# Optimization experiments

Hardware: AMD Instinct MI355X
Metric: run time of the kernel (lower is better)

The kernel has to match this reference:

```python
import jax, jax.numpy as jnp
import numpy as np

N_NODES = 100000
N_EDGES = 800000
NODE_F = 32
EDGE_F = 16
HID = 128
EPS = 1e-5


def _bn(h, g, b):
    # BatchNorm1d in training mode: biased batch stats over dim 0
    m = h.mean(axis=0)
    v = jnp.mean((h - m) ** 2, axis=0)
    return (h - m) * jax.lax.rsqrt(v + EPS) * g + b


def _sage(x, src, dst, Wl, bl, Wr):
    # PyG SAGEConv (mean aggr): lin_l(mean_{j->i} x_j) + lin_r(x_i)
    s = jax.ops.segment_sum(x[src], dst, num_segments=N_NODES)
    cnt = jax.ops.segment_sum(jnp.ones((src.shape[0], 1), x.dtype), dst, num_segments=N_NODES)
    mean = s / jnp.maximum(cnt, 1.0)
    return mean @ Wl + bl + x @ Wr


def setup_inputs() -> dict:
    key = jax.random.key(0)
    ks = jax.random.split(key, 32)

    def lin(k, fi, fo):
        return jax.random.normal(k, (fi, fo), jnp.float32) / np.sqrt(fi)

    inp = {
        'x': jax.random.normal(ks[0], (N_NODES, NODE_F), jnp.float32),
        'edge_index': jax.random.randint(ks[1], (2, N_EDGES), 0, N_NODES),
        'edge_attr': jax.random.normal(ks[2], (N_EDGES, EDGE_F), jnp.float32),
        'edge_source': jax.random.randint(ks[3], (N_EDGES,), 0, N_NODES),
        'edge_target': jax.random.randint(ks[4], (N_EDGES,), 0, N_NODES),
        'W1l': lin(ks[5], NODE_F, HID), 'b1': jnp.zeros((HID,), jnp.float32), 'W1r': lin(ks[6], NODE_F, HID),
        'W2l': lin(ks[7], HID, HID), 'b2': jnp.zeros((HID,), jnp.float32), 'W2r': lin(ks[8], HID, HID),
        'bn1_g': jnp.ones((HID,), jnp.float32), 'bn1_b': jnp.zeros((HID,), jnp.float32),
        'bn2_g': jnp.ones((HID,), jnp.float32), 'bn2_b': jnp.zeros((HID,), jnp.float32),
        'We': lin(ks[9], EDGE_F, HID), 'be': jnp.zeros((HID,), jnp.float32),
        'bne_g': jnp.ones((HID,), jnp.float32), 'bne_b': jnp.zeros((HID,), jnp.float32),
        'Wm1': lin(ks[10], 3 * HID, HID), 'bm1': jnp.zeros((HID,), jnp.float32),
        'bnm_g': jnp.ones((HID,), jnp.float32), 'bnm_b': jnp.zeros((HID,), jnp.float32),
        'Wm2': lin(ks[11], HID, HID // 2), 'bm2': jnp.zeros((HID // 2,), jnp.float32),
        'Wm3': lin(ks[12], HID // 2, 1), 'bm3': jnp.zeros((1,), jnp.float32),
    }
    return inp


def reference(x, edge_index, edge_attr, edge_source, edge_target,
              W1l, b1, W1r, W2l, b2, W2r, bn1_g, bn1_b, bn2_g, bn2_b,
              We, be, bne_g, bne_b, Wm1, bm1, bnm_g, bnm_b, Wm2, bm2, Wm3, bm3):
    src, dst = edge_index[0], edge_index[1]
    h = jax.nn.relu(_bn(_sage(x, src, dst, W1l, b1, W1r), bn1_g, bn1_b))  # dropout = identity (eval)
    h = jax.nn.relu(_bn(_sage(h, src, dst, W2l, b2, W2r), bn2_g, bn2_b))
    ef = _bn(jax.nn.relu(edge_attr @ We + be), bne_g, bne_b)  # Linear->ReLU->BN->Dropout(id)
    z = jnp.concatenate([h[edge_source], h[edge_target], ef], axis=1)  # [E, 3*HID]
    z = _bn(jax.nn.relu(z @ Wm1 + bm1), bnm_g, bnm_b)
    z = jax.nn.relu(z @ Wm2 + bm2)
    return (z @ Wm3 + bm3).squeeze(-1)
```

## Files before the change

kernel.cpp:

```cpp
#include <hip/hip_runtime.h>
#include <hip/hip_bf16.h>

#define NN 100000
#define NE 800000
#define SCAN_NB 98

typedef __attribute__((ext_vector_type(8))) short bf16x8;
typedef __attribute__((ext_vector_type(4))) float f32x4;

__device__ __forceinline__ short f2b(float f) {
    unsigned u = __float_as_uint(f);
    unsigned r = (u + 0x7fffu + ((u >> 16) & 1u)) >> 16;
    return (short)r;
}
__device__ __forceinline__ float b2f(short s) {
    return __uint_as_float(((unsigned)(unsigned short)s) << 16);
}
__device__ __forceinline__ unsigned cvt2(float a, float b) {
    unsigned r;
    asm("v_cvt_pk_bf16_f32 %0, %1, %2" : "=v"(r) : "v"(a), "v"(b));
    return r;
}
__device__ __forceinline__ float blo(unsigned u) { return __uint_as_float(u << 16); }
__device__ __forceinline__ float bhi(unsigned u) { return __uint_as_float(u & 0xffff0000u); }

__global__ __launch_bounds__(256) void k_prep_hist(
    const float* __restrict__ We, const float* __restrict__ Wm1,
    const float* __restrict__ W2l, const float* __restrict__ W2r,
    short* __restrict__ WteT, short* __restrict__ WmsT,
    short* __restrict__ WmdT, short* __restrict__ W2cT,
    const int* __restrict__ ei, int* __restrict__ deg)
{
    int b = blockIdx.x;
    int tid = threadIdx.x;
    if (b >= 5) {
        int e = (b - 5) * 256 + tid;
        if (e < NE) atomicAdd(&deg[ei[NE + e]], 1);
        return;
    }
    if (tid >= 128) return;
    int j = tid;
    if (b == 0) {
        for (int k = 0; k < 32; k++)
            WteT[j * 32 + k] = (k < 16) ? f2b(We[k * 128 + j]) : (short)0;
    } else if (b == 1) {
        for (int k = 0; k < 128; k++) WmsT[j * 128 + k] = f2b(Wm1[k * 128 + j]);
    } else if (b == 2) {
        for (int k = 0; k < 128; k++) WmdT[j * 128 + k] = f2b(Wm1[(128 + k) * 128 + j]);
    } else if (b == 3) {
        for (int k = 0; k < 128; k++) W2cT[j * 256 + k] = f2b(W2l[k * 128 + j]);
    } else {
        for (int k = 0; k < 128; k++) W2cT[j * 256 + 128 + k] = f2b(W2r[k * 128 + j]);
    }
}

__global__ __launch_bounds__(1024) void k_scan_a(const int* __restrict__ deg,
    int* __restrict__ tmp, int* __restrict__ bsum)
{
    __shared__ int sh[1024];
    int t = threadIdx.x, b = blockIdx.x;
    int idx = b * 1024 + t;
    int v = (idx < NN) ? deg[idx] : 0;
    sh[t] = v;
    __syncthreads();
    for (int ofs = 1; ofs < 1024; ofs <<= 1) {
        int u = (t >= ofs) ? sh[t - ofs] : 0;
        __syncthreads();
        sh[t] += u;
        __syncthreads();
    }
    if (idx < NN) tmp[idx] = sh[t] - v;
    if (t == 1023) bsum[b] = sh[1023];
}

__global__ void k_scan_b(const int* __restrict__ bsum, int* __restrict__ boff,
    int* __restrict__ rowptr)
{
    if (threadIdx.x == 0) {
        int acc = 0;
        for (int i = 0; i < SCAN_NB; i++) { boff[i] = acc; acc += bsum[i]; }
        rowptr[NN] = acc;
    }
}

__global__ __launch_bounds__(1024) void k_scan_c(const int* __restrict__ tmp,
    const int* __restrict__ boff, int* __restrict__ rowptr, int* __restrict__ wp)
{
    int b = blockIdx.x, t = threadIdx.x;
    int idx = b * 1024 + t;
    if (idx < NN) {
        int v = boff[b] + tmp[idx];
        rowptr[idx] = v; wp[idx] = v;
    }
}

#define SCAT_NB 3125
__global__ __launch_bounds__(256) void k_scat_e0(
    const int* __restrict__ ei, int* __restrict__ wp, int* __restrict__ elist,
    const float* __restrict__ ea, const short* __restrict__ WteT, const float* __restrict__ be,
    float* __restrict__ ssum, float* __restrict__ ssq)
{
    const int tid = threadIdx.x;
    if (blockIdx.x < SCAT_NB) {
        int e = blockIdx.x * 256 + tid;
        if (e < NE) {
            int d = ei[NE + e];
            int pos = atomicAdd(&wp[d], 1);
            elist[pos] = ei[e];
        }
        return;
    }
    __shared__ float sRed[2][128];
    const int wave = tid >> 6, lane = tid & 63;
    const int quad = lane >> 4, ln = lane & 15;
    const int waveM = wave >> 1, waveN = wave & 1;
    const int colbase = 64 * waveN, row16 = 16 * waveM;
    if (tid < 128) { sRed[0][tid] = 0.f; sRed[1][tid] = 0.f; }

    bf16x8 bWe[4];
    float bec[4];
    #pragma unroll
    for (int nt = 0; nt < 4; nt++) {
        bWe[nt] = *(const bf16x8*)(WteT + (colbase + nt * 16 + ln) * 32 + quad * 8);
        bec[nt] = be[colbase + nt * 16 + ln];
    }
    float s1[4] = {0,0,0,0}, s2[4] = {0,0,0,0};
    f32x4 zero = {0.f, 0.f, 0.f, 0.f};
    __syncthreads();

    const int G = gridDim.x - SCAT_NB;
    const int NT = NE / 32;
    float4 fe0 = {0,0,0,0}, fe1 = {0,0,0,0};
    int t = blockIdx.x - SCAT_NB;
    if (t < NT && quad < 2) {
        const float* p = ea + (size_t)(t * 32 + row16 + ln) * 16 + quad * 8;
        fe0 = *(const float4*)p; fe1 = *(const float4*)(p + 4);
    }
    for (; t < NT; t += G) {
        bf16x8 aE;
        if (quad < 2) {
            uint4 uw;
            uw.x = cvt2(fe0.x, fe0.y); uw.y = cvt2(fe0.z, fe0.w);
            uw.z = cvt2(fe1.x, fe1.y); uw.w = cvt2(fe1.z, fe1.w);
            aE = *(bf16x8*)&uw;
        } else {
            #pragma unroll
            for (int i = 0; i < 8; i++) aE[i] = 0;
        }
        int t1 = t + G;
        if (t1 < NT && quad < 2) {
            const float* p = ea + (size_t)(t1 * 32 + row16 + ln) * 16 + quad * 8;
            fe0 = *(const float4*)p; fe1 = *(const float4*)(p + 4);
        }
        f32x4 tacc[4];
        #pragma unroll
        for (int nt = 0; nt < 4; nt++)
            tacc[nt] = __builtin_amdgcn_mfma_f32_16x16x32_bf16(aE, bWe[nt], zero, 0, 0, 0);
        #pragma unroll
        for (int nt = 0; nt < 4; nt++)
            #pragma unroll
            for (int r = 0; r < 4; r++) {
                float v = fmaxf(tacc[nt][r] + bec[nt], 0.f);
                s1[nt] += v; s2[nt] += v * v;
            }
    }
    #pragma unroll
    for (int nt = 0; nt < 4; nt++) {
        float a1 = s1[nt], a2 = s2[nt];
        a1 += __shfl_down(a1, 32); a1 += __shfl_down(a1, 16);
        a2 += __shfl_down(a2, 32); a2 += __shfl_down(a2, 16);
        if (quad == 0) {
            atomicAdd(&sRed[0][colbase + nt * 16 + ln], a1);
            atomicAdd(&sRed[1][colbase + nt * 16 + ln], a2);
        }
    }
    __syncthreads();
    if (tid < 128) {
        atomicAdd(&ssum[tid], sRed[0][tid]);
        atomicAdd(&ssq[tid],  sRed[1][tid]);
    }
}

__global__ __launch_bounds__(256) void k_gagg1f(const float* __restrict__ x,
    const int* __restrict__ rowptr, const int* __restrict__ elist, float* __restrict__ meanX,
    const float* __restrict__ essum, const float* __restrict__ essq,
    const float* __restrict__ bne_g, const float* __restrict__ bne_b,
    const float* __restrict__ Wm1, const float* __restrict__ bm1,
    short* __restrict__ W1pT, float* __restrict__ bm1p)
{
    if (blockIdx.x == NN / 8) {
        __shared__ float sa[128], scc[128];
        int tid = threadIdx.x;
        if (tid < 128) {
            float m = essum[tid] / (float)NE;
            float var = essq[tid] / (float)NE - m * m;
            float rs = rsqrtf(var + 1e-5f);
            float a = bne_g[tid] * rs;
            sa[tid] = a; scc[tid] = bne_b[tid] - m * a;
        }
        __syncthreads();
        if (tid < 128) {
            float acc = bm1[tid];
            for (int k = 0; k < 128; k++) {
                float w = Wm1[(256 + k) * 128 + tid];
                W1pT[tid * 128 + k] = f2b(sa[k] * w);
                acc += scc[k] * w;
            }
            bm1p[tid] = acc;
        }
        return;
    }
    int n = blockIdx.x * 8 + (threadIdx.x >> 5);
    int j = threadIdx.x & 31;
    int b = rowptr[n], e = rowptr[n + 1];
    float acc = 0.f;
    int i = b;
    for (; i + 4 <= e; i += 4) {
        int s0 = elist[i], s1 = elist[i + 1], s2 = elist[i + 2], s3 = elist[i + 3];
        float a0 = x[(size_t)s0 * 32 + j];
        float a1 = x[(size_t)s1 * 32 + j];
        float a2 = x[(size_t)s2 * 32 + j];
        float a3 = x[(size_t)s3 * 32 + j];
        acc += (a0 + a1) + (a2 + a3);
    }
    for (; i < e; i++) acc += x[(size_t)elist[i] * 32 + j];
    float inv = (e > b) ? 1.0f / (float)(e - b) : 1.0f;
    meanX[(size_t)n * 32 + j] = acc * inv;
}

__global__ __launch_bounds__(256) void k_gagg2(const short* __restrict__ h1b,
    const int* __restrict__ rowptr, const int* __restrict__ elist,
    const float* __restrict__ ssum1, const float* __restrict__ ssq1,
    const float* __restrict__ g1, const float* __restrict__ b1g, short* __restrict__ m2b)
{
    int n = blockIdx.x * 8 + (threadIdx.x >> 5);
    int c0 = (threadIdx.x & 31) * 4;
    float sc[4], sh[4];
    #pragma unroll
    for (int i = 0; i < 4; i++) {
        float m = ssum1[c0 + i] / (float)NN;
        float var = ssq1[c0 + i] / (float)NN - m * m;
        float rs = rsqrtf(var + 1e-5f);
        float s = g1[c0 + i] * rs;
        sc[i] = s; sh[i] = b1g[c0 + i] - m * s;
    }
    int b = rowptr[n], e = rowptr[n + 1];
    float acc[4] = {0.f, 0.f, 0.f, 0.f};
    int i = b;
    for (; i + 4 <= e; i += 4) {
        int s0 = elist[i], s1 = elist[i + 1], s2 = elist[i + 2], s3 = elist[i + 3];
        uint2 u0 = *(const uint2*)(h1b + (size_t)s0 * 128 + c0);
        uint2 u1 = *(const uint2*)(h1b + (size_t)s1 * 128 + c0);
        uint2 u2 = *(const uint2*)(h1b + (size_t)s2 * 128 + c0);
        uint2 u3 = *(const uint2*)(h1b + (size_t)s3 * 128 + c0);
        acc[0] += fmaxf(blo(u0.x) * sc[0] + sh[0], 0.f) + fmaxf(blo(u1.x) * sc[0] + sh[0], 0.f)
                + fmaxf(blo(u2.x) * sc[0] + sh[0], 0.f) + fmaxf(blo(u3.x) * sc[0] + sh[0], 0.f);
        acc[1] += fmaxf(bhi(u0.x) * sc[1] + sh[1], 0.f) + fmaxf(bhi(u1.x) * sc[1] + sh[1], 0.f)
                + fmaxf(bhi(u2.x) * sc[1] + sh[1], 0.f) + fmaxf(bhi(u3.x) * sc[1] + sh[1], 0.f);
        acc[2] += fmaxf(blo(u0.y) * sc[2] + sh[2], 0.f) + fmaxf(blo(u1.y) * sc[2] + sh[2], 0.f)
                + fmaxf(blo(u2.y) * sc[2] + sh[2], 0.f) + fmaxf(blo(u3.y) * sc[2] + sh[2], 0.f);
        acc[3] += fmaxf(bhi(u0.y) * sc[3] + sh[3], 0.f) + fmaxf(bhi(u1.y) * sc[3] + sh[3], 0.f)
                + fmaxf(bhi(u2.y) * sc[3] + sh[3], 0.f) + fmaxf(bhi(u3.y) * sc[3] + sh[3], 0.f);
    }
    for (; i < e; i++) {
        int s = elist[i];
        uint2 u = *(const uint2*)(h1b + (size_t)s * 128 + c0);
        acc[0] += fmaxf(blo(u.x) * sc[0] + sh[0], 0.f);
        acc[1] += fmaxf(bhi(u.x) * sc[1] + sh[1], 0.f);
        acc[2] += fmaxf(blo(u.y) * sc[2] + sh[2], 0.f);
        acc[3] += fmaxf(bhi(u.y) * sc[3] + sh[3], 0.f);
    }
    float inv = (e > b) ? 1.0f / (float)(e - b) : 1.0f;
    uint2 ow;
    ow.x = cvt2(acc[0] * inv, acc[1] * inv);
    ow.y = cvt2(acc[2] * inv, acc[3] * inv);
    *(uint2*)(m2b + (size_t)n * 128 + c0) = ow;
}

__global__ __launch_bounds__(256) void k_node_l1(
    const float* __restrict__ meanX, const float* __restrict__ x,
    const float* __restrict__ Wl, const float* __restrict__ Wr,
    const float* __restrict__ bias,
    short* __restrict__ outp, float* __restrict__ ssum, float* __restrict__ ssq)
{
    __shared__ __align__(16) float sWl[32][128];
    __shared__ __align__(16) float sWr[32][128];
    __shared__ __align__(16) float sA[32][36];
    __shared__ __align__(16) float sB[32][36];
    __shared__ float red[2][128], red2[2][128];
    int tid = threadIdx.x;
    int j = tid & 127, rg = tid >> 7;
    int r0 = blockIdx.x * 32;

    for (int f = tid * 4; f < 4096; f += 1024) {
        *(float4*)((float*)sWl + f) = *(const float4*)(Wl + f);
        *(float4*)((float*)sWr + f) = *(const float4*)(Wr + f);
    }
    {
        int r = tid >> 3, c = (tid & 7) * 4;
        *(float4*)(&sA[r][c]) = *(const float4*)(meanX + (size_t)(r0 + r) * 32 + c);
        *(float4*)(&sB[r][c]) = *(const float4*)(x + (size_t)(r0 + r) * 32 + c);
    }
    __syncthreads();

    float acc[16];
    #pragma unroll
    for (int r = 0; r < 16; r++) acc[r] = 0.0f;
    int rb = rg * 16;
    #pragma unroll
    for (int kq = 0; kq < 8; kq++) {
        int k = kq * 4;
        float wl0 = sWl[k][j], wl1 = sWl[k+1][j], wl2 = sWl[k+2][j], wl3 = sWl[k+3][j];
        float wr0 = sWr[k][j], wr1 = sWr[k+1][j], wr2 = sWr[k+2][j], wr3 = sWr[k+3][j];
        #pragma unroll
        for (int r = 0; r < 16; r++) {
            float4 a = *(float4*)(&sA[rb + r][k]);
            float4 b = *(float4*)(&sB[rb + r][k]);
            acc[r] += a.x*wl0 + a.y*wl1 + a.z*wl2 + a.w*wl3
                    + b.x*wr0 + b.y*wr1 + b.z*wr2 + b.w*wr3;
        }
    }
    float bj = bias[j];
    float s1 = 0.0f, s2 = 0.0f;
    #pragma unroll
    for (int r = 0; r < 16; r += 2) {
        float v0 = acc[r] + bj, v1 = acc[r + 1] + bj;
        s1 += v0 + v1; s2 += v0 * v0 + v1 * v1;
        unsigned p = cvt2(v0, v1);
        outp[(size_t)(r0 + rb + r) * 128 + j]     = (short)p;
        outp[(size_t)(r0 + rb + r + 1) * 128 + j] = (short)(p >> 16);
    }
    red[rg][j] = s1; red2[rg][j] = s2;
    __syncthreads();
    if (rg == 0) {
        atomicAdd(&ssum[j], red[0][j] + red[1][j]);
        atomicAdd(&ssq[j],  red2[0][j] + red2[1][j]);
    }
}

__global__ __launch_bounds__(256) void k_node_l2m(
    const short* __restrict__ m2b, const short* __restrict__ h1b,
    const float* __restrict__ ssum1, const float* __restrict__ ssq1,
    const float* __restrict__ g1, const float* __restrict__ b1g,
    const short* __restrict__ W2cT, const float* __restrict__ bias,
    short* __restrict__ h2b, float* __restrict__ ssum, float* __restrict__ ssq)
{
    __shared__ __align__(16) short sK[32][264];
    __shared__ float sRed[2][128];
    __shared__ float sS[128], sH[128];
    const int tid = threadIdx.x;
    const int wave = tid >> 6, lane = tid & 63, quad = lane >> 4, ln = lane & 15;
    const int waveM = wave >> 1, waveN = wave & 1;
    const int colbase = 64 * waveN, row16 = 16 * waveM;
    if (tid < 128) {
        float m = ssum1[tid] / (float)NN;
        float var = ssq1[tid] / (float)NN - m * m;
        float rs = rsqrtf(var + 1e-5f);
        float s = g1[tid] * rs;
        sS[tid] = s; sH[tid] = b1g[tid] - m * s;
        sRed[0][tid] = 0.f; sRed[1][tid] = 0.f;
    }

    bf16x8 bW[4][8];
    #pragma unroll
    for (int nt = 0; nt < 4; nt++)
        #pragma unroll
        for (int kk = 0; kk < 8; kk++)
            bW[nt][kk] = *(const bf16x8*)(W2cT + (size_t)(colbase + nt * 16 + ln) * 256 + kk * 32 + quad * 8);
    float bc[4];
    #pragma unroll
    for (int nt = 0; nt < 4; nt++) bc[nt] = bias[colbase + nt * 16 + ln];

    float s1[4] = {0,0,0,0}, s2[4] = {0,0,0,0};
    f32x4 zero = {0.f, 0.f, 0.f, 0.f};
    __syncthreads();

    for (int t = blockIdx.x; t < NN / 32; t += gridDim.x) {
        int r0 = t * 32;
        __syncthreads();
        {
            int r = tid >> 3, seg = tid & 7;
            if (seg < 4) {
                const bf16x8* src = (const bf16x8*)(m2b + (size_t)(r0 + r) * 128 + seg * 32);
                bf16x8* dst = (bf16x8*)(&sK[r][seg * 32]);
                dst[0] = src[0]; dst[1] = src[1]; dst[2] = src[2]; dst[3] = src[3];
            } else {
                int c0 = (seg - 4) * 32;
                const uint4* pw = (const uint4*)(h1b + (size_t)(r0 + r) * 128 + c0);
                uint4* dw = (uint4*)(&sK[r][128 + c0]);
                #pragma unroll
                for (int i2 = 0; i2 < 4; i2++) {
                    uint4 u = pw[i2];
                    int cb = c0 + i2 * 8;
                    uint4 ow;
                    ow.x = cvt2(fmaxf(blo(u.x)*sS[cb+0]+sH[cb+0],0.f), fmaxf(bhi(u.x)*sS[cb+1]+sH[cb+1],0.f));
                    ow.y = cvt2(fmaxf(blo(u.y)*sS[cb+2]+sH[cb+2],0.f), fmaxf(bhi(u.y)*sS[cb+3]+sH[cb+3],0.f));
                    ow.z = cvt2(fmaxf(blo(u.z)*sS[cb+4]+sH[cb+4],0.f), fmaxf(bhi(u.z)*sS[cb+5]+sH[cb+5],0.f));
                    ow.w = cvt2(fmaxf(blo(u.w)*sS[cb+6]+sH[cb+6],0.f), fmaxf(bhi(u.w)*sS[cb+7]+sH[cb+7],0.f));
                    dw[i2] = ow;
                }
            }
        }
        __syncthreads();
        f32x4 acc[4] = {zero, zero, zero, zero};
        #pragma unroll
        for (int kk = 0; kk < 8; kk++) {
            bf16x8 a = *(const bf16x8*)(&sK[row16 + ln][kk * 32 + quad * 8]);
            #pragma unroll
            for (int nt = 0; nt < 4; nt++)
                acc[nt] = __builtin_amdgcn_mfma_f32_16x16x32_bf16(a, bW[nt][kk], acc[nt], 0, 0, 0);
        }
        #pragma unroll
        for (int nt = 0; nt < 4; nt++) {
            int col = colbase + nt * 16 + ln;
            float v0 = acc[nt][0] + bc[nt], v1 = acc[nt][1] + bc[nt];
            float v2 = acc[nt][2] + bc[nt], v3 = acc[nt][3] + bc[nt];
            s1[nt] += (v0 + v1) + (v2 + v3);
            s2[nt] += (v0*v0 + v1*v1) + (v2*v2 + v3*v3);
            unsigned p01 = cvt2(v0, v1), p23 = cvt2(v2, v3);
            h2b[(size_t)(r0 + row16 + quad * 4 + 0) * 128 + col] = (short)p01;
            h2b[(size_t)(r0 + row16 + quad * 4 + 1) * 128 + col] = (short)(p01 >> 16);
            h2b[(size_t)(r0 + row16 + quad * 4 + 2) * 128 + col] = (short)p23;
            h2b[(size_t)(r0 + row16 + quad * 4 + 3) * 128 + col] = (short)(p23 >> 16);
        }
    }
    #pragma unroll
    for (int nt = 0; nt < 4; nt++) {
        float a1 = s1[nt], a2 = s2[nt];
        a1 += __shfl_down(a1, 32); a1 += __shfl_down(a1, 16);
        a2 += __shfl_down(a2, 32); a2 += __shfl_down(a2, 16);
        if (quad == 0) {
            atomicAdd(&sRed[0][colbase + nt * 16 + ln], a1);
            atomicAdd(&sRed[1][colbase + nt * 16 + ln], a2);
        }
    }
    __syncthreads();
    if (tid < 128) {
        atomicAdd(&ssum[tid], sRed[0][tid]);
        atomicAdd(&ssq[tid],  sRed[1][tid]);
    }
}

__global__ __launch_bounds__(256) void k_proj_mfma(
    const short* __restrict__ h2b,
    const float* __restrict__ ssum2, const float* __restrict__ ssq2,
    const float* __restrict__ g2, const float* __restrict__ b2g,
    const short* __restrict__ WT0, const short* __restrict__ WT1,
    short* __restrict__ C0, short* __restrict__ C1)
{
    __shared__ __align__(16) short sA[32][136];
    __shared__ float sS[128], sH[128];
    const int tid = threadIdx.x;
    const int wave = tid >> 6, lane = tid & 63, quad = lane >> 4, ln = lane & 15;
    const int waveM = wave >> 1, waveN = wave & 1;
    const int colbase = 64 * waveN, row16 = 16 * waveM;
    const int half = (blockIdx.x >= 512) ? 1 : 0;
    const short* WT = half ? WT1 : WT0;
    short* C = half ? C1 : C0;
    const int b0 = blockIdx.x - half * 512;
    if (tid < 128) {
        float m = ssum2[tid] / (float)NN;
        float var = ssq2[tid] / (float)NN - m * m;
        float rs = rsqrtf(var + 1e-5f);
        float s = g2[tid] * rs;
        sS[tid] = s; sH[tid] = b2g[tid] - m * s;
    }
    bf16x8 bW[4][4];
    #pragma unroll
    for (int nt = 0; nt < 4; nt++)
        #pragma unroll
        for (int kk = 0; kk < 4; kk++)
            bW[nt][kk] = *(const bf16x8*)(WT + (colbase + nt * 16 + ln) * 128 + kk * 32 + quad * 8);
    f32x4 zero = {0.f, 0.f, 0.f, 0.f};
    __syncthreads();
    for (int t = b0; t < NN / 32; t += 512) {
        int r0 = t * 32;
        __syncthreads();
        {
            int r = tid >> 3, c0 = (tid & 7) * 16;
            const uint4* pw = (const uint4*)(h2b + (size_t)(r0 + r) * 128 + c0);
            uint4* dw = (uint4*)(&sA[r][c0]);
            #pragma unroll
            for (int i2 = 0; i2 < 2; i2++) {
                uint4 u = pw[i2];
                int cb = c0 + i2 * 8;
                uint4 ow;
                ow.x = cvt2(fmaxf(blo(u.x)*sS[cb+0]+sH[cb+0],0.f), fmaxf(bhi(u.x)*sS[cb+1]+sH[cb+1],0.f));
                ow.y = cvt2(fmaxf(blo(u.y)*sS[cb+2]+sH[cb+2],0.f), fmaxf(bhi(u.y)*sS[cb+3]+sH[cb+3],0.f));
                ow.z = cvt2(fmaxf(blo(u.z)*sS[cb+4]+sH[cb+4],0.f), fmaxf(bhi(u.z)*sS[cb+5]+sH[cb+5],0.f));
                ow.w = cvt2(fmaxf(blo(u.w)*sS[cb+6]+sH[cb+6],0.f), fmaxf(bhi(u.w)*sS[cb+7]+sH[cb+7],0.f));
                dw[i2] = ow;
            }
        }
        __syncthreads();
        f32x4 acc[4] = {zero, zero, zero, zero};
        #pragma unroll
        for (int kk = 0; kk < 4; kk++) {
            bf16x8 a = *(const bf16x8*)(&sA[row16 + ln][kk * 32 + quad * 8]);
            #pragma unroll
            for (int nt = 0; nt < 4; nt++)
                acc[nt] = __builtin_amdgcn_mfma_f32_16x16x32_bf16(a, bW[nt][kk], acc[nt], 0, 0, 0);
        }
        #pragma unroll
        for (int nt = 0; nt < 4; nt++) {
            int col = colbase + nt * 16 + ln;
            unsigned p01 = cvt2(acc[nt][0], acc[nt][1]);
            unsigned p23 = cvt2(acc[nt][2], acc[nt][3]);
            C[(size_t)(r0 + row16 + quad * 4 + 0) * 128 + col] = (short)p01;
            C[(size_t)(r0 + row16 + quad * 4 + 1) * 128 + col] = (short)(p01 >> 16);
            C[(size_t)(r0 + row16 + quad * 4 + 2) * 128 + col] = (short)p23;
            C[(size_t)(r0 + row16 + quad * 4 + 3) * 128 + col] = (short)(p23 >> 16);
        }
    }
}

__global__ __launch_bounds__(512) void k_edge_m1(
    const float* __restrict__ ea,
    const short* __restrict__ WteT, const float* __restrict__ be,
    const short* __restrict__ W1pT, const float* __restrict__ bm1p,
    const short* __restrict__ hs, const short* __restrict__ hd,
    const int* __restrict__ esrc, const int* __restrict__ etgt,
    float* __restrict__ ssum, float* __restrict__ ssq,
    short* __restrict__ vbuf)
{
    __shared__ __align__(16) short sT[64][136];
    __shared__ __align__(16) float sSum[64][132];
    __shared__ float sRed[2][128];

    const int tid = threadIdx.x;
    const int wave = tid >> 6, lane = tid & 63;
    const int quad = lane >> 4, ln = lane & 15;
    const int waveM = wave >> 1, waveN = wave & 1;
    const int colbase = 64 * waveN, row16 = 16 * waveM;

    if (tid < 128) { sRed[0][tid] = 0.f; sRed[1][tid] = 0.f; }

    bf16x8 bWe[4], bW1[4][4];
    float bec[4], bmc[4];
    #pragma unroll
    for (int nt = 0; nt < 4; nt++) {
        bWe[nt] = *(const bf16x8*)(WteT + (colbase + nt * 16 + ln) * 32 + quad * 8);
        #pragma unroll
        for (int kk = 0; kk < 4; kk++)
            bW1[nt][kk] = *(const bf16x8*)(W1pT + (colbase + nt * 16 + ln) * 128 + kk * 32 + quad * 8);
        bec[nt] = be[colbase + nt * 16 + ln];
        bmc[nt] = bm1p[colbase + nt * 16 + ln];
    }

    const int srow = tid >> 4;
    const int scol = (tid & 15) * 8;

    float s1[4] = {0,0,0,0}, s2[4] = {0,0,0,0};
    f32x4 zero = {0.f, 0.f, 0.f, 0.f};

    const int G = gridDim.x;
    const int NT = NE / 64;
    bf16x8 gA = {}, gB = {}, gC = {}, gD = {};
    int i1sA = 0, i1tA = 0, i1sB = 0, i1tB = 0;
    float4 fe0 = {0,0,0,0}, fe1 = {0,0,0,0};

    int t = blockIdx.x;
    if (t < NT) {
        const int e0 = t * 64;
        int s0 = esrc[e0 + srow],       d0 = etgt[e0 + srow];
        int s1i = esrc[e0 + srow + 32], d1 = etgt[e0 + srow + 32];
        gA = *(const bf16x8*)(hs + (size_t)s0 * 128 + scol);
        gB = *(const bf16x8*)(hd + (size_t)d0 * 128 + scol);
        gC = *(const bf16x8*)(hs + (size_t)s1i * 128 + scol);
        gD = *(const bf16x8*)(hd + (size_t)d1 * 128 + scol);
        int t1 = t + G;
        if (t1 < NT) {
            i1sA = esrc[t1 * 64 + srow];      i1tA = etgt[t1 * 64 + srow];
            i1sB = esrc[t1 * 64 + srow + 32]; i1tB = etgt[t1 * 64 + srow + 32];
        }
        if (quad < 2) {
            const float* p = ea + (size_t)(e0 + row16 + ln) * 16 + quad * 8;
            fe0 = *(const float4*)p; fe1 = *(const float4*)(p + 4);
        }
    }

    for (; t < NT; t += G) {
        const int e0 = t * 64;

        bf16x8 aE;
        if (quad < 2) {
            uint4 uw;
            uw.x = cvt2(fe0.x, fe0.y); uw.y = cvt2(fe0.z, fe0.w);
            uw.z = cvt2(fe1.x, fe1.y); uw.w = cvt2(fe1.z, fe1.w);
            aE = *(bf16x8*)&uw;
        } else {
            #pragma unroll
            for (int i = 0; i < 8; i++) aE[i] = 0;
        }
        f32x4 tacc[4];
        #pragma unroll
        for (int nt = 0; nt < 4; nt++)
            tacc[nt] = __builtin_amdgcn_mfma_f32_16x16x32_bf16(aE, bWe[nt], zero, 0, 0, 0);

        __syncthreads();

        #pragma unroll
        for (int nt = 0; nt < 4; nt++) {
            int col = colbase + nt * 16 + ln;
            unsigned p01 = cvt2(fmaxf(tacc[nt][0] + bec[nt], 0.f), fmaxf(tacc[nt][1] + bec[nt], 0.f));
            unsigned p23 = cvt2(fmaxf(tacc[nt][2] + bec[nt], 0.f), fmaxf(tacc[nt][3] + bec[nt], 0.f));
            sT[row16 + quad * 4 + 0][col] = (short)p01;
            sT[row16 + quad * 4 + 1][col] = (short)(p01 >> 16);
            sT[row16 + quad * 4 + 2][col] = (short)p23;
            sT[row16 + quad * 4 + 3][col] = (short)(p23 >> 16);
        }
        {
            uint4 uA = *(const uint4*)&gA, uB = *(const uint4*)&gB;
            uint4 uC = *(const uint4*)&gC, uD = *(const uint4*)&gD;
            f32x4 a0, a1, b0, b1;
            a0[0] = blo(uA.x) + blo(uB.x); a0[1] = bhi(uA.x) + bhi(uB.x);
            a0[2] = blo(uA.y) + blo(uB.y); a0[3] = bhi(uA.y) + bhi(uB.y);
            a1[0] = blo(uA.z) + blo(uB.z); a1[1] = bhi(uA.z) + bhi(uB.z);
            a1[2] = blo(uA.w) + blo(uB.w); a1[3] = bhi(uA.w) + bhi(uB.w);
            b0[0] = blo(uC.x) + blo(uD.x); b0[1] = bhi(uC.x) + bhi(uD.x);
            b0[2] = blo(uC.y) + blo(uD.y); b0[3] = bhi(uC.y) + bhi(uD.y);
            b1[0] = blo(uC.z) + blo(uD.z); b1[1] = bhi(uC.z) + bhi(uD.z);
            b1[2] = blo(uC.w) + blo(uD.w); b1[3] = bhi(uC.w) + bhi(uD.w);
            *(f32x4*)(&sSum[srow][scol])          = a0;
            *(f32x4*)(&sSum[srow][scol + 4])      = a1;
            *(f32x4*)(&sSum[srow + 32][scol])     = b0;
            *(f32x4*)(&sSum[srow + 32][scol + 4]) = b1;
        }
        {
            int t1 = t + G;
            if (t1 < NT) {
                gA = *(const bf16x8*)(hs + (size_t)i1sA * 128 + scol);
                gB = *(const bf16x8*)(hd + (size_t)i1tA * 128 + scol);
                gC = *(const bf16x8*)(hs + (size_t)i1sB * 128 + scol);
                gD = *(const bf16x8*)(hd + (size_t)i1tB * 128 + scol);
                int t2 = t1 + G;
                if (t2 < NT) {
                    i1sA = esrc[t2 * 64 + srow];      i1tA = etgt[t2 * 64 + srow];
                    i1sB = esrc[t2 * 64 + srow + 32]; i1tB = etgt[t2 * 64 + srow + 32];
                }
                if (quad < 2) {
                    const float* p = ea + (size_t)(t1 * 64 + row16 + ln) * 16 + quad * 8;
                    fe0 = *(const float4*)p; fe1 = *(const float4*)(p + 4);
                }
            }
        }
        __syncthreads();

        f32x4 uacc[4] = {zero, zero, zero, zero};
        #pragma unroll
        for (int kk = 0; kk < 4; kk++) {
            bf16x8 aU = *(const bf16x8*)(&sT[row16 + ln][kk * 32 + quad * 8]);
            #pragma unroll
            for (int nt = 0; nt < 4; nt++)
                uacc[nt] = __builtin_amdgcn_mfma_f32_16x16x32_bf16(aU, bW1[nt][kk], uacc[nt], 0, 0, 0);
        }
        #pragma unroll
        for (int nt = 0; nt < 4; nt++) {
            int col = colbase + nt * 16 + ln;
            float v0 = fmaxf(uacc[nt][0] + bmc[nt] + sSum[row16 + quad * 4 + 0][col], 0.f);
            float v1 = fmaxf(uacc[nt][1] + bmc[nt] + sSum[row16 + quad * 4 + 1][col], 0.f);
            float v2 = fmaxf(uacc[nt][2] + bmc[nt] + sSum[row16 + quad * 4 + 2][col], 0.f);
            float v3 = fmaxf(uacc[nt][3] + bmc[nt] + sSum[row16 + quad * 4 + 3][col], 0.f);
            s1[nt] += (v0 + v1) + (v2 + v3);
            s2[nt] += (v0*v0 + v1*v1) + (v2*v2 + v3*v3);
            unsigned p01 = cvt2(v0, v1), p23 = cvt2(v2, v3);
            vbuf[(size_t)(e0 + row16 + quad * 4 + 0) * 128 + col] = (short)p01;
            vbuf[(size_t)(e0 + row16 + quad * 4 + 1) * 128 + col] = (short)(p01 >> 16);
            vbuf[(size_t)(e0 + row16 + quad * 4 + 2) * 128 + col] = (short)p23;
            vbuf[(size_t)(e0 + row16 + quad * 4 + 3) * 128 + col] = (short)(p23 >> 16);
        }
    }

    #pragma unroll
    for (int nt = 0; nt < 4; nt++) {
        float a1 = s1[nt], a2 = s2[nt];
        a1 += __shfl_down(a1, 32); a1 += __shfl_down(a1, 16);
        a2 += __shfl_down(a2, 32); a2 += __shfl_down(a2, 16);
        if (quad == 0) {
            atomicAdd(&sRed[0][colbase + nt * 16 + ln], a1);
            atomicAdd(&sRed[1][colbase + nt * 16 + ln], a2);
        }
    }
    __syncthreads();
    if (tid < 128) {
        atomicAdd(&ssum[tid], sRed[0][tid]);
        atomicAdd(&ssq[tid],  sRed[1][tid]);
    }
}

// ... 26 lines not shown
    if (MODE < 2) {
        if (tid < 128) { sRed[0][tid] = 0.f; sRed[1][tid] = 0.f; }
    }
    float b2c[2] = {0.f, 0.f};
    if (MODE >= 2) {
        float* sSc   = (float*)sZ;
        float* sSh   = sSc + 128;
        float* sPart = sSh + 128;
        float* sB2   = sPart + 256;
        if (tid < 128) {
            float m = ssum[tid] / (float)NE;
            float var = ssq[tid] / (float)NE - m * m;
            float rs = rsqrtf(var + 1e-5f);
            float a = bnm_g[tid] * rs;
            sSc[tid] = a; sSh[tid] = bnm_b[tid] - m * a;
        }
        if (tid < 64) sW3[tid] = Wm3[tid];
        __syncthreads();
        {
            int col = tid & 63, kg = tid >> 6;
            float acc = 0.f;
            for (int k = kg * 32; k < kg * 32 + 32; k++) {
                float w = Wm2[k * 64 + col];
                sW2[col][k] = f2b(sSc[k] * w);
                acc += sSh[k] * w;
            }
            sPart[kg * 64 + col] = acc;
        }
        __syncthreads();
        if (tid < 64)
            ((float*)sZ)[512 + tid] = bm2[tid] + sPart[tid] + sPart[64 + tid]
                                    + sPart[128 + tid] + sPart[192 + tid];
        __syncthreads();
        b2c[0] = sB2[32 * waveN + ln];
        b2c[1] = sB2[32 * waveN + 16 + ln];
    }

    bf16x8 bWe[4], bW1[4][4];
    if (MODE <= 2) {
        #pragma unroll
        for (int nt = 0; nt < 4; nt++) {
            bWe[nt] = *(const bf16x8*)(WteT + (colbase + nt * 16 + ln) * 32 + quad * 8);
            if (MODE >= 1) {
                #pragma unroll
                for (int kk = 0; kk < 4; kk++)
                    bW1[nt][kk] = *(const bf16x8*)(W1pT + (colbase + nt * 16 + ln) * 128 + kk * 32 + quad * 8);
            }
        }
    }
    float bec[4], bmc[4];
    #pragma unroll
    for (int nt = 0; nt < 4; nt++) {
        bec[nt] = (MODE <= 2) ? be[colbase + nt * 16 + ln] : 0.f;
        bmc[nt] = (MODE == 1 || MODE == 2) ? bm1p[colbase + nt * 16 + ln] : 0.f;
    }
    float bm3v = (MODE >= 2) ? bm3[0] : 0.f;

    const int srow = tid >> 4;
    const int scol = (tid & 15) * 8;

    float s1[4] = {0,0,0,0}, s2[4] = {0,0,0,0};
    f32x4 zero = {0.f, 0.f, 0.f, 0.f};
    __syncthreads();

    if constexpr (MODE == 3) {
        const int G = gridDim.x;
        const int NT = NE / 32;
        bf16x8 aV0 = {}, aV1 = {}, aV2 = {}, aV3 = {};
        int t = blockIdx.x;
        if (t < NT) {
            const short* p = vbuf + (size_t)(t * 32 + row16 + ln) * 128 + quad * 8;
            aV0 = *(const bf16x8*)(p);
            aV1 = *(const bf16x8*)(p + 32);
            aV2 = *(const bf16x8*)(p + 64);
            aV3 = *(const bf16x8*)(p + 96);
        }
        for (; t < NT; t += G) {
            const int e0 = t * 32;
            f32x4 vacc[2] = {zero, zero};
            #pragma unroll
            for (int n2 = 0; n2 < 2; n2++) {
                bf16x8 bV0 = *(const bf16x8*)(&sW2[32 * waveN + n2 * 16 + ln][0 * 32 + quad * 8]);
                bf16x8 bV1 = *(const bf16x8*)(&sW2[32 * waveN + n2 * 16 + ln][1 * 32 + quad * 8]);
                bf16x8 bV2 = *(const bf16x8*)(&sW2[32 * waveN + n2 * 16 + ln][2 * 32 + quad * 8]);
                bf16x8 bV3 = *(const bf16x8*)(&sW2[32 * waveN + n2 * 16 + ln][3 * 32 + quad * 8]);
                vacc[n2] = __builtin_amdgcn_mfma_f32_16x16x32_bf16(aV0, bV0, vacc[n2], 0, 0, 0);
                vacc[n2] = __builtin_amdgcn_mfma_f32_16x16x32_bf16(aV1, bV1, vacc[n2], 0, 0, 0);
                vacc[n2] = __builtin_amdgcn_mfma_f32_16x16x32_bf16(aV2, bV2, vacc[n2], 0, 0, 0);
                vacc[n2] = __builtin_amdgcn_mfma_f32_16x16x32_bf16(aV3, bV3, vacc[n2], 0, 0, 0);
            }
            {
                int t1 = t + G;
                if (t1 < NT) {
                    const short* p = vbuf + (size_t)(t1 * 32 + row16 + ln) * 128 + quad * 8;
                    aV0 = *(const bf16x8*)(p);
                    aV1 = *(const bf16x8*)(p + 32);
                    aV2 = *(const bf16x8*)(p + 64);
                    aV3 = *(const bf16x8*)(p + 96);
                }
            }
            __syncthreads();
            #pragma unroll
            for (int n2 = 0; n2 < 2; n2++) {
                int col2 = 32 * waveN + n2 * 16 + ln;
                #pragma unroll
                for (int r = 0; r < 4; r++)
                    sZ[row16 + quad * 4 + r][col2] = fmaxf(vacc[n2][r] + b2c[n2], 0.f);
            }
            __syncthreads();
            {
                int row = wave * 8 + (lane >> 3);
                int ks  = (lane & 7) * 8;
                float o = 0.f;
                #pragma unroll
                for (int k2 = 0; k2 < 8; k2++)
                    o += sZ[row][ks + k2] * sW3[ks + k2];
                o += __shfl_xor(o, 1);
                o += __shfl_xor(o, 2);
                o += __shfl_xor(o, 4);
                if ((lane & 7) == 0) outp[e0 + row] = o + bm3v;
            }
        }
    } else if constexpr (MODE == 2) {
    for (int t = blockIdx.x; t < NE / 32; t += gridDim.x) {
        const int e0 = t * 32;

        int isA = esrc[e0 + srow],      itA = etgt[e0 + srow];
        int isB = esrc[e0 + srow + 16], itB = etgt[e0 + srow + 16];

        bf16x8 aE;
        if (quad < 2) {
            const float* p = ea + (size_t)(e0 + row16 + ln) * 16 + quad * 8;
            float4 f0 = *(const float4*)p, f1 = *(const float4*)(p + 4);
            uint4 uw;
            uw.x = cvt2(f0.x, f0.y); uw.y = cvt2(f0.z, f0.w);
            uw.z = cvt2(f1.x, f1.y); uw.w = cvt2(f1.z, f1.w);
            aE = *(bf16x8*)&uw;
        } else {
            #pragma unroll
            for (int i = 0; i < 8; i++) aE[i] = 0;
        }
        f32x4 tacc[4];
        #pragma unroll
        for (int nt = 0; nt < 4; nt++)
            tacc[nt] = __builtin_amdgcn_mfma_f32_16x16x32_bf16(aE, bWe[nt], zero, 0, 0, 0);

        __syncthreads();
        {
            bf16x8 gA = *(const bf16x8*)(hs + (size_t)isA * 128 + scol);
            bf16x8 gB = *(const bf16x8*)(hd + (size_t)itA * 128 + scol);
            bf16x8 gC = *(const bf16x8*)(hs + (size_t)isB * 128 + scol);
            bf16x8 gD = *(const bf16x8*)(hd + (size_t)itB * 128 + scol);
            #pragma unroll
            for (int nt = 0; nt < 4; nt++) {
                int col = colbase + nt * 16 + ln;
                unsigned p01 = cvt2(fmaxf(tacc[nt][0] + bec[nt], 0.f), fmaxf(tacc[nt][1] + bec[nt], 0.f));
                unsigned p23 = cvt2(fmaxf(tacc[nt][2] + bec[nt], 0.f), fmaxf(tacc[nt][3] + bec[nt], 0.f));
                sT[row16 + quad * 4 + 0][col] = (short)p01;
                sT[row16 + quad * 4 + 1][col] = (short)(p01 >> 16);
                sT[row16 + quad * 4 + 2][col] = (short)p23;
                sT[row16 + quad * 4 + 3][col] = (short)(p23 >> 16);
            }
            uint4 uA = *(const uint4*)&gA, uB = *(const uint4*)&gB;
            uint4 uC = *(const uint4*)&gC, uD = *(const uint4*)&gD;
            f32x4 a0, a1, b0, b1;
            a0[0] = blo(uA.x) + blo(uB.x); a0[1] = bhi(uA.x) + bhi(uB.x);
            a0[2] = blo(uA.y) + blo(uB.y); a0[3] = bhi(uA.y) + bhi(uB.y);
            a1[0] = blo(uA.z) + blo(uB.z); a1[1] = bhi(uA.z) + bhi(uB.z);
            a1[2] = blo(uA.w) + blo(uB.w); a1[3] = bhi(uA.w) + bhi(uB.w);
            b0[0] = blo(uC.x) + blo(uD.x); b0[1] = bhi(uC.x) + bhi(uD.x);
            b0[2] = blo(uC.y) + blo(uD.y); b0[3] = bhi(uC.y) + bhi(uD.y);
            b1[0] = blo(uC.z) + blo(uD.z); b1[1] = bhi(uC.z) + bhi(uD.z);
            b1[2] = blo(uC.w) + blo(uD.w); b1[3] = bhi(uC.w) + bhi(uD.w);
            *(f32x4*)(&sSum[srow][scol])          = a0;
            *(f32x4*)(&sSum[srow][scol + 4])      = a1;
            *(f32x4*)(&sSum[srow + 16][scol])     = b0;
            *(f32x4*)(&sSum[srow + 16][scol + 4]) = b1;
        }
        __syncthreads();

        f32x4 uacc[4] = {zero, zero, zero, zero};
        #pragma unroll
        for (int kk = 0; kk < 4; kk++) {
            bf16x8 aU = *(const bf16x8*)(&sT[row16 + ln][kk * 32 + quad * 8]);
            #pragma unroll
            for (int nt = 0; nt < 4; nt++)
                uacc[nt] = __builtin_amdgcn_mfma_f32_16x16x32_bf16(aU, bW1[nt][kk], uacc[nt], 0, 0, 0);
        }

        __syncthreads();
        #pragma unroll
        for (int nt = 0; nt < 4; nt++) {
            int col = colbase + nt * 16 + ln;
            #pragma unroll
            for (int r = 0; r < 4; r++) {
                float v = uacc[nt][r] + bmc[nt] + sSum[row16 + quad * 4 + r][col];
                sT[row16 + quad * 4 + r][col] = f2b(fmaxf(v, 0.f));
            }
        }
        __syncthreads();
        f32x4 vacc[2] = {zero, zero};
        #pragma unroll
        for (int kk = 0; kk < 4; kk++) {
            bf16x8 aV = *(const bf16x8*)(&sT[row16 + ln][kk * 32 + quad * 8]);
            #pragma unroll
            for (int n2 = 0; n2 < 2; n2++) {
                bf16x8 bV = *(const bf16x8*)(&sW2[32 * waveN + n2 * 16 + ln][kk * 32 + quad * 8]);
                vacc[n2] = __builtin_amdgcn_mfma_f32_16x16x32_bf16(aV, bV, vacc[n2], 0, 0, 0);
            }
        }
        #pragma unroll
        for (int n2 = 0; n2 < 2; n2++) {
            int col2 = 32 * waveN + n2 * 16 + ln;
            #pragma unroll
            for (int r = 0; r < 4; r++)
                sZ[row16 + quad * 4 + r][col2] = fmaxf(vacc[n2][r] + b2c[n2], 0.f);
        }
        __syncthreads();
        {
            int row = wave * 8 + (lane >> 3);
            int ks  = (lane & 7) * 8;
            float o = 0.f;
            #pragma unroll
            for (int k2 = 0; k2 < 8; k2++)
                o += sZ[row][ks + k2] * sW3[ks + k2];
            o += __shfl_xor(o, 1);
            o += __shfl_xor(o, 2);
            o += __shfl_xor(o, 4);
            if ((lane & 7) == 0) outp[e0 + row] = o + bm3v;
        }
    }
    }

    if (MODE < 2) {
        #pragma unroll
        for (int nt = 0; nt < 4; nt++) {
            float a1 = s1[nt], a2 = s2[nt];
            a1 += __shfl_down(a1, 32); a1 += __shfl_down(a1, 16);
            a2 += __shfl_down(a2, 32); a2 += __shfl_down(a2, 16);
            if (quad == 0) {
                atomicAdd(&sRed[0][colbase + nt * 16 + ln], a1);
                atomicAdd(&sRed[1][colbase + nt * 16 + ln], a2);
            }
        }
        __syncthreads();
        if (tid < 128) {
            atomicAdd(&ssum[tid], sRed[0][tid]);
            atomicAdd(&ssq[tid],  sRed[1][tid]);
        }
    }
}

extern "C" void kernel_launch(void* const* d_in, const int* in_sizes, int n_in,
                              void* d_out, int out_size, void* d_ws, size_t ws_size,
                              hipStream_t stream) {
    const float* x     = (const float*)d_in[0];
    const int*   ei    = (const int*)  d_in[1];
    const float* eattr = (const float*)d_in[2];
    const int*   esrc  = (const int*)  d_in[3];
    const int*   etgt  = (const int*)  d_in[4];
    const float* W1l = (const float*)d_in[5];  const float* b1 = (const float*)d_in[6];
    const float* W1r = (const float*)d_in[7];
    const float* W2l = (const float*)d_in[8];  const float* b2 = (const float*)d_in[9];
    const float* W2r = (const float*)d_in[10];
    const float* bn1_g = (const float*)d_in[11]; const float* bn1_b = (const float*)d_in[12];
    const float* bn2_g = (const float*)d_in[13]; const float* bn2_b = (const float*)d_in[14];
    const float* We  = (const float*)d_in[15]; const float* be  = (const float*)d_in[16];
    const float* bne_g = (const float*)d_in[17]; const float* bne_b = (const float*)d_in[18];
    const float* Wm1 = (const float*)d_in[19]; const float* bm1 = (const float*)d_in[20];
    const float* bnm_g = (const float*)d_in[21]; const float* bnm_b = (const float*)d_in[22];
    const float* Wm2 = (const float*)d_in[23]; const float* bm2 = (const float*)d_in[24];
    const float* Wm3 = (const float*)d_in[25]; const float* bm3 = (const float*)d_in[26];
    float* out = (float*)d_out;

    char* base = (char*)d_ws;
    size_t o = 0;
    auto A = [&](size_t bytes) { char* p = base + o; o = (o + bytes + 255) & ~(size_t)255; return p; };
    short* hsb   = (short*)A((size_t)NN * 128 * 2);
    short* hdb   = (short*)A((size_t)NN * 128 * 2);
    int*   deg   = (int*)  A((size_t)NN * 4);
    int*   rowptr= (int*)  A((size_t)(NN + 1) * 4);
    int*   wp    = (int*)  A((size_t)NN * 4);
    int*   elist = (int*)  A((size_t)NE * 4);
    float* st    = (float*)A(1024 * 4);
    int*   bsum  = (int*)  A(SCAN_NB * 4);
    int*   boff  = (int*)  A(SCAN_NB * 4);
    float* sc1   = (float*)A(512); float* sh1 = (float*)A(512);
    float* sc2   = (float*)A(512); float* sh2 = (float*)A(512);
    float* bm1p  = (float*)A(512); float* b2p = (float*)A(256);
    short* WteT  = (short*)A(128 * 32 * 2);
    short* W1pT  = (short*)A(128 * 128 * 2);
    short* WmsT  = (short*)A(128 * 128 * 2);
    short* WmdT  = (short*)A(128 * 128 * 2);
    short* W2pT  = (short*)A(64 * 128 * 2);
    short* W2cT  = (short*)A(128 * 256 * 2);
    size_t chain = o;
    float* meanX = (float*)A((size_t)NN * 32 * 4);
    short* h1b   = (short*)A((size_t)NN * 128 * 2);
    short* m2b   = (short*)A((size_t)NN * 128 * 2);
    short* h2b   = (short*)A((size_t)NN * 128 * 2);
    int*   stmp  = (int*)meanX;
    short* vbuf  = (short*)(base + chain);
    bool storev = ws_size >= chain + (size_t)NE * 128 * 2;
    (void)W2pT; (void)b2p; (void)sc1; (void)sh1; (void)sc2; (void)sh2;

    hipMemsetAsync(deg, 0, (size_t)NN * 4, stream);
    hipMemsetAsync(st, 0, 1024 * 4, stream);

    k_prep_hist<<<5 + (NE + 255) / 256, 256, 0, stream>>>(We, Wm1, W2l, W2r,
        WteT, WmsT, WmdT, W2cT, ei, deg);
    k_scan_a<<<SCAN_NB, 1024, 0, stream>>>(deg, stmp, bsum);
    k_scan_b<<<1, 64, 0, stream>>>(bsum, boff, rowptr);
    k_scan_c<<<SCAN_NB, 1024, 0, stream>>>(stmp, boff, rowptr, wp);

    k_scat_e0<<<SCAT_NB + 2048, 256, 0, stream>>>(ei, wp, elist,
        eattr, WteT, be, st + 512, st + 640);

    k_gagg1f<<<NN / 8 + 1, 256, 0, stream>>>(x, rowptr, elist, meanX,
        st + 512, st + 640, bne_g, bne_b, Wm1, bm1, W1pT, bm1p);
    k_node_l1<<<NN / 32, 256, 0, stream>>>(meanX, x, W1l, W1r, b1, h1b, st + 0, st + 128);

    k_gagg2<<<NN / 8, 256, 0, stream>>>(h1b, rowptr, elist, st + 0, st + 128, bn1_g, bn1_b, m2b);
    k_node_l2m<<<512, 256, 0, stream>>>(m2b, h1b, st + 0, st + 128, bn1_g, bn1_b,
        W2cT, b2, h2b, st + 256, st + 384);

    k_proj_mfma<<<1024, 256, 0, stream>>>(h2b, st + 256, st + 384, bn2_g, bn2_b,
        WmsT, WmdT, hsb, hdb);

    if (storev)
        k_edge_m1<<<512, 512, 0, stream>>>(eattr, WteT, be, W1pT, bm1p, hsb, hdb,
            esrc, etgt, st + 768, st + 896, vbuf);
    else
        k_edge_mfma<2><<<1024, 256, 0, stream>>>(eattr, WteT, be, W1pT, bm1p, hsb, hdb,
            esrc, etgt, Wm2, bm2, bnm_g, bnm_b, Wm3, bm3, st + 768, st + 896, nullptr, out);

    if (storev)
        k_edge_mfma<3><<<1536, 256, 0, stream>>>(eattr, WteT, be, W1pT, bm1p, hsb, hdb,
            esrc, etgt, Wm2, bm2, bnm_g, bnm_b, Wm3, bm3, st + 768, st + 896, vbuf, out);
}
```

Baseline: 710.6 us.

## Fuse neighbor mean aggregation into SAGE layer GEMM kernels

The two gather-mean kernels (layer-1 on x, layer-2 on BN+ReLU of h1) are folded into the node linear kernels. Each block now computes its 32 rows of neighbor means directly into shared memory, so the meanX and m2b intermediate buffers are no longer written and re-read, and two launches go away. The trade-off is that the latency-bound gather now runs inside the GEMM blocks, which may lower occupancy or serialize gather and compute. k_node_l2mf is persistent with only 512 blocks, so the gather parallelism there is reduced.

```diff
diff --git a/kernel.cpp b/kernel.cpp
--- a/kernel.cpp
+++ b/kernel.cpp
@@ -181,14 +181,18 @@
     }
 }
 
-__global__ __launch_bounds__(256) void k_gagg1f(const float* __restrict__ x,
-    const int* __restrict__ rowptr, const int* __restrict__ elist, float* __restrict__ meanX,
+__global__ __launch_bounds__(256) void k_node_l1f(
+    const float* __restrict__ x,
+    const int* __restrict__ rowptr, const int* __restrict__ elist,
+    const float* __restrict__ Wl, const float* __restrict__ Wr,
+    const float* __restrict__ bias,
     const float* __restrict__ essum, const float* __restrict__ essq,
     const float* __restrict__ bne_g, const float* __restrict__ bne_b,
     const float* __restrict__ Wm1, const float* __restrict__ bm1,
-    short* __restrict__ W1pT, float* __restrict__ bm1p)
+    short* __restrict__ W1pT, float* __restrict__ bm1p,
+    short* __restrict__ outp, float* __restrict__ ssum, float* __restrict__ ssq)
 {
-    if (blockIdx.x == NN / 8) {
+    if (blockIdx.x == NN / 32) {
         __shared__ float sa[128], scc[128];
         int tid = threadIdx.x;
         if (tid < 128) {
@@ -210,79 +214,6 @@
         }
         return;
     }
-    int n = blockIdx.x * 8 + (threadIdx.x >> 5);
-    int j = threadIdx.x & 31;
-    int b = rowptr[n], e = rowptr[n + 1];
-    float acc = 0.f;
-    int i = b;
-    for (; i + 4 <= e; i += 4) {
-        int s0 = elist[i], s1 = elist[i + 1], s2 = elist[i + 2], s3 = elist[i + 3];
-        float a0 = x[(size_t)s0 * 32 + j];
-        float a1 = x[(size_t)s1 * 32 + j];
-        float a2 = x[(size_t)s2 * 32 + j];
-        float a3 = x[(size_t)s3 * 32 + j];
-        acc += (a0 + a1) + (a2 + a3);
-    }
-    for (; i < e; i++) acc += x[(size_t)elist[i] * 32 + j];
-    float inv = (e > b) ? 1.0f / (float)(e - b) : 1.0f;
-    meanX[(size_t)n * 32 + j] = acc * inv;
-}
-
-__global__ __launch_bounds__(256) void k_gagg2(const short* __restrict__ h1b,
-    const int* __restrict__ rowptr, const int* __restrict__ elist,
-    const float* __restrict__ ssum1, const float* __restrict__ ssq1,
-    const float* __restrict__ g1, const float* __restrict__ b1g, short* __restrict__ m2b)
-{
-    int n = blockIdx.x * 8 + (threadIdx.x >> 5);
-    int c0 = (threadIdx.x & 31) * 4;
-    float sc[4], sh[4];
-    #pragma unroll
-    for (int i = 0; i < 4; i++) {
-        float m = ssum1[c0 + i] / (float)NN;
-        float var = ssq1[c0 + i] / (float)NN - m * m;
-        float rs = rsqrtf(var + 1e-5f);
-        float s = g1[c0 + i] * rs;
-        sc[i] = s; sh[i] = b1g[c0 + i] - m * s;
-    }
-    int b = rowptr[n], e = rowptr[n + 1];
-    float acc[4] = {0.f, 0.f, 0.f, 0.f};
-    int i = b;
-    for (; i + 4 <= e; i += 4) {
-        int s0 = elist[i], s1 = elist[i + 1], s2 = elist[i + 2], s3 = elist[i + 3];
-        uint2 u0 = *(const uint2*)(h1b + (size_t)s0 * 128 + c0);
-        uint2 u1 = *(const uint2*)(h1b + (size_t)s1 * 128 + c0);
-        uint2 u2 = *(const uint2*)(h1b + (size_t)s2 * 128 + c0);
-        uint2 u3 = *(const uint2*)(h1b + (size_t)s3 * 128 + c0);
-        acc[0] += fmaxf(blo(u0.x) * sc[0] + sh[0], 0.f) + fmaxf(blo(u1.x) * sc[0] + sh[0], 0.f)
-                + fmaxf(blo(u2.x) * sc[0] + sh[0], 0.f) + fmaxf(blo(u3.x) * sc[0] + sh[0], 0.f);
-        acc[1] += fmaxf(bhi(u0.x) * sc[1] + sh[1], 0.f) + fmaxf(bhi(u1.x) * sc[1] + sh[1], 0.f)
-                + fmaxf(bhi(u2.x) * sc[1] + sh[1], 0.f) + fmaxf(bhi(u3.x) * sc[1] + sh[1], 0.f);
-        acc[2] += fmaxf(blo(u0.y) * sc[2] + sh[2], 0.f) + fmaxf(blo(u1.y) * sc[2] + sh[2], 0.f)
-                + fmaxf(blo(u2.y) * sc[2] + sh[2], 0.f) + fmaxf(blo(u3.y) * sc[2] + sh[2], 0.f);
-        acc[3] += fmaxf(bhi(u0.y) * sc[3] + sh[3], 0.f) + fmaxf(bhi(u1.y) * sc[3] + sh[3], 0.f)
-                + fmaxf(bhi(u2.y) * sc[3] + sh[3], 0.f) + fmaxf(bhi(u3.y) * sc[3] + sh[3], 0.f);
-    }
-    for (; i < e; i++) {
-        int s = elist[i];
-        uint2 u = *(const uint2*)(h1b + (size_t)s * 128 + c0);
-        acc[0] += fmaxf(blo(u.x) * sc[0] + sh[0], 0.f);
-        acc[1] += fmaxf(bhi(u.x) * sc[1] + sh[1], 0.f);
-        acc[2] += fmaxf(blo(u.y) * sc[2] + sh[2], 0.f);
-        acc[3] += fmaxf(bhi(u.y) * sc[3] + sh[3], 0.f);
-    }
-    float inv = (e > b) ? 1.0f / (float)(e - b) : 1.0f;
-    uint2 ow;
-    ow.x = cvt2(acc[0] * inv, acc[1] * inv);
-    ow.y = cvt2(acc[2] * inv, acc[3] * inv);
-    *(uint2*)(m2b + (size_t)n * 128 + c0) = ow;
-}
-
-__global__ __launch_bounds__(256) void k_node_l1(
-    const float* __restrict__ meanX, const float* __restrict__ x,
-    const float* __restrict__ Wl, const float* __restrict__ Wr,
-    const float* __restrict__ bias,
-    short* __restrict__ outp, float* __restrict__ ssum, float* __restrict__ ssq)
-{
     __shared__ __align__(16) float sWl[32][128];
     __shared__ __align__(16) float sWr[32][128];
     __shared__ __align__(16) float sA[32][36];
@@ -298,8 +229,29 @@
     }
     {
         int r = tid >> 3, c = (tid & 7) * 4;
-        *(float4*)(&sA[r][c]) = *(const float4*)(meanX + (size_t)(r0 + r) * 32 + c);
         *(float4*)(&sB[r][c]) = *(const float4*)(x + (size_t)(r0 + r) * 32 + c);
+    }
+    {
+        int nl = tid >> 5;
+        int jj = tid & 31;
+        #pragma unroll
+        for (int pass = 0; pass < 4; pass++) {
+            int n = r0 + pass * 8 + nl;
+            int b = rowptr[n], e = rowptr[n + 1];
+            float acc = 0.f;
+            int i = b;
+            for (; i + 4 <= e; i += 4) {
+                int s0 = elist[i], s1 = elist[i + 1], s2 = elist[i + 2], s3 = elist[i + 3];
+                float a0 = x[(size_t)s0 * 32 + jj];
+                float a1 = x[(size_t)s1 * 32 + jj];
+                float a2 = x[(size_t)s2 * 32 + jj];
+                float a3 = x[(size_t)s3 * 32 + jj];
+                acc += (a0 + a1) + (a2 + a3);
+            }
+            for (; i < e; i++) acc += x[(size_t)elist[i] * 32 + jj];
+            float inv = (e > b) ? 1.0f / (float)(e - b) : 1.0f;
+            sA[pass * 8 + nl][jj] = acc * inv;
+        }
     }
     __syncthreads();
 
@@ -338,8 +290,9 @@
     }
 }
 
-__global__ __launch_bounds__(256) void k_node_l2m(
-    const short* __restrict__ m2b, const short* __restrict__ h1b,
+__global__ __launch_bounds__(256) void k_node_l2mf(
+    const short* __restrict__ h1b,
+    const int* __restrict__ rowptr, const int* __restrict__ elist,
     const float* __restrict__ ssum1, const float* __restrict__ ssq1,
     const float* __restrict__ g1, const float* __restrict__ b1g,
     const short* __restrict__ W2cT, const float* __restrict__ bias,
@@ -375,16 +328,53 @@
     f32x4 zero = {0.f, 0.f, 0.f, 0.f};
     __syncthreads();
 
+    const int gnl = tid >> 5;
+    const int gc0 = (tid & 31) * 4;
+    float gsc[4], gsh[4];
+    #pragma unroll
+    for (int i = 0; i < 4; i++) { gsc[i] = sS[gc0 + i]; gsh[i] = sH[gc0 + i]; }
+
     for (int t = blockIdx.x; t < NN / 32; t += gridDim.x) {
         int r0 = t * 32;
         __syncthreads();
+        #pragma unroll
+        for (int pass = 0; pass < 4; pass++) {
+            int n = r0 + pass * 8 + gnl;
+            int b = rowptr[n], e = rowptr[n + 1];
+            float acc[4] = {0.f, 0.f, 0.f, 0.f};
+            int i = b;
+            for (; i + 4 <= e; i += 4) {
+                int s0i = elist[i], s1i = elist[i + 1], s2i = elist[i + 2], s3i = elist[i + 3];
+                uint2 u0 = *(const uint2*)(h1b + (size_t)s0i * 128 + gc0);
+                uint2 u1 = *(const uint2*)(h1b + (size_t)s1i * 128 + gc0);
+                uint2 u2 = *(const uint2*)(h1b + (size_t)s2i * 128 + gc0);
+                uint2 u3 = *(const uint2*)(h1b + (size_t)s3i * 128 + gc0);
+                acc[0] += fmaxf(blo(u0.x) * gsc[0] + gsh[0], 0.f) + fmaxf(blo(u1.x) * gsc[0] + gsh[0], 0.f)
+                        + fmaxf(blo(u2.x) * gsc[0] + gsh[0], 0.f) + fmaxf(blo(u3.x) * gsc[0] + gsh[0], 0.f);
+                acc[1] += fmaxf(bhi(u0.x) * gsc[1] + gsh[1], 0.f) + fmaxf(bhi(u1.x) * gsc[1] + gsh[1], 0.f)
+                        + fmaxf(bhi(u2.x) * gsc[1] + gsh[1], 0.f) + fmaxf(bhi(u3.x) * gsc[1] + gsh[1], 0.f);
+                acc[2] += fmaxf(blo(u0.y) * gsc[2] + gsh[2], 0.f) + fmaxf(blo(u1.y) * gsc[2] + gsh[2], 0.f)
+                        + fmaxf(blo(u2.y) * gsc[2] + gsh[2], 0.f) + fmaxf(blo(u3.y) * gsc[2] + gsh[2], 0.f);
+                acc[3] += fmaxf(bhi(u0.y) * gsc[3] + gsh[3], 0.f) + fmaxf(bhi(u1.y) * gsc[3] + gsh[3], 0.f)
+                        + fmaxf(bhi(u2.y) * gsc[3] + gsh[3], 0.f) + fmaxf(bhi(u3.y) * gsc[3] + gsh[3], 0.f);
+            }
+            for (; i < e; i++) {
+                int s = elist[i];
+                uint2 u = *(const uint2*)(h1b + (size_t)s * 128 + gc0);
+                acc[0] += fmaxf(blo(u.x) * gsc[0] + gsh[0], 0.f);
+                acc[1] += fmaxf(bhi(u.x) * gsc[1] + gsh[1], 0.f);
+                acc[2] += fmaxf(blo(u.y) * gsc[2] + gsh[2], 0.f);
+                acc[3] += fmaxf(bhi(u.y) * gsc[3] + gsh[3], 0.f);
+            }
+            float inv = (e > b) ? 1.0f / (float)(e - b) : 1.0f;
+            uint2 ow;
+            ow.x = cvt2(acc[0] * inv, acc[1] * inv);
+            ow.y = cvt2(acc[2] * inv, acc[3] * inv);
+            *(uint2*)(&sK[pass * 8 + gnl][gc0]) = ow;
+        }
         {
             int r = tid >> 3, seg = tid & 7;
-            if (seg < 4) {
-                const bf16x8* src = (const bf16x8*)(m2b + (size_t)(r0 + r) * 128 + seg * 32);
-                bf16x8* dst = (bf16x8*)(&sK[r][seg * 32]);
-                dst[0] = src[0]; dst[1] = src[1]; dst[2] = src[2]; dst[3] = src[3];
-            } else {
+            if (seg >= 4) {
                 int c0 = (seg - 4) * 32;
                 const uint4* pw = (const uint4*)(h1b + (size_t)(r0 + r) * 128 + c0);
                 uint4* dw = (uint4*)(&sK[r][128 + c0]);
@@ -1017,7 +1007,7 @@
     int*   stmp  = (int*)meanX;
     short* vbuf  = (short*)(base + chain);
     bool storev = ws_size >= chain + (size_t)NE * 128 * 2;
-    (void)W2pT; (void)b2p; (void)sc1; (void)sh1; (void)sc2; (void)sh2;
+    (void)W2pT; (void)b2p; (void)sc1; (void)sh1; (void)sc2; (void)sh2; (void)m2b; (void)meanX;
 
     hipMemsetAsync(deg, 0, (size_t)NN * 4, stream);
     hipMemsetAsync(st, 0, 1024 * 4, stream);
@@ -1031,13 +1021,12 @@
     k_scat_e0<<<SCAT_NB + 2048, 256, 0, stream>>>(ei, wp, elist,
         eattr, WteT, be, st + 512, st + 640);
 
-    k_gagg1f<<<NN / 8 + 1, 256, 0, stream>>>(x, rowptr, elist, meanX,
-        st + 512, st + 640, bne_g, bne_b, Wm1, bm1, W1pT, bm1p);
-    k_node_l1<<<NN / 32, 256, 0, stream>>>(meanX, x, W1l, W1r, b1, h1b, st + 0, st + 128);
-
-    k_gagg2<<<NN / 8, 256, 0, stream>>>(h1b, rowptr, elist, st + 0, st + 128, bn1_g, bn1_b, m2b);
-    k_node_l2m<<<512, 256, 0, stream>>>(m2b, h1b, st + 0, st + 128, bn1_g, bn1_b,
-        W2cT, b2, h2b, st + 256, st + 384);
+    k_node_l1f<<<NN / 32 + 1, 256, 0, stream>>>(x, rowptr, elist, W1l, W1r, b1,
+        st + 512, st + 640, bne_g, bne_b, Wm1, bm1, W1pT, bm1p,
+        h1b, st + 0, st + 128);
+
+    k_node_l2mf<<<512, 256, 0, stream>>>(h1b, rowptr, elist,
+        st + 0, st + 128, bn1_g, bn1_b, W2cT, b2, h2b, st + 256, st + 384);
 
     k_proj_mfma<<<1024, 256, 0, stream>>>(h2b, st + 256, st + 384, bn2_g, bn2_b,
         WmsT, WmdT, hsb, hdb);
```

After: 832.6 us. 1.17x slower.
